# Kernel optimization log

Hardware: AMD Instinct MI355X
Metric: run time of the kernel (lower is better)

Reference implementation:

```python
import jax, jax.numpy as jnp
import numpy as np

S, B, E, H = 2048, 2, 1024, 16
D = E // H


def setup_inputs() -> dict:
    key = jax.random.key(0)
    k1, k2, k3, k4 = jax.random.split(key, 4)
    x = jax.random.normal(k1, (S, B, E), dtype=jnp.float32)
    # xavier_uniform for [3E, E] and [O, E]
    lim_qkv = float(np.sqrt(6.0 / (3 * E + E)))
    lim_out = float(np.sqrt(6.0 / (E + E)))
    w_qkv = jax.random.uniform(k2, (3 * E, E), jnp.float32, -lim_qkv, lim_qkv)
    b_qkv = jnp.zeros((3 * E,), jnp.float32)
    w_out = jax.random.uniform(k3, (E, E), jnp.float32, -lim_out, lim_out)
    b_out = jnp.zeros((E,), jnp.float32)
    return {"x": x, "w_qkv": w_qkv, "b_qkv": b_qkv, "w_out": w_out, "b_out": b_out}


def reference(x, w_qkv, b_qkv, w_out, b_out):
    # x: [S, B, E] (seq-first, as in the torch module)
    s, b, e = x.shape
    scaling = jnp.asarray(np.sqrt(D), x.dtype)
    qkv = jnp.einsum('sbe,fe->sbf', x, w_qkv) + b_qkv          # [S,B,3E]
    q, k, v = jnp.split(qkv, 3, axis=-1)
    q = q.reshape(s, b, H, D)
    k = k.reshape(s, b, H, D)
    v = v.reshape(s, b, H, D)
    # scores [B,H,S,S]; note original divides by sqrt(head_dim)
    scores = jnp.einsum('sbhd,tbhd->bhst', q, k) / scaling
    attn_w = jax.nn.softmax(scores.astype(jnp.float32), axis=-1).astype(scores.dtype)
    # dropout p=0.1 is identity in eval mode (training=False)
    attn = jnp.einsum('bhst,tbhd->sbhd', attn_w, v).reshape(s, b, e)
    out = jnp.einsum('sbe,oe->sbo', attn, w_out) + b_out        # [S,B,O]
    attn_avg = attn_w.mean(axis=1)                              # [B,S,S]
    return out, attn_avg
```

## Files before the change

### kernel.cpp

```cpp
#include <hip/hip_runtime.h>

#define SEQ   2048
#define BATCH 2
#define NH    16
#define HD    64
#define EMB   1024

#define QSCALE 0.18033688011112042f

using bf16x8 = __attribute__((ext_vector_type(8))) short;
using f32x4  = __attribute__((ext_vector_type(4))) float;
using f32x16 = __attribute__((ext_vector_type(16))) float;

__device__ __forceinline__ unsigned short f2bf(float f) {
  unsigned int u = __float_as_uint(f);
  u += 0x7FFFu + ((u >> 16) & 1u);
  return (unsigned short)(u >> 16);
}
__device__ __forceinline__ unsigned pk_bf16(float lo, float hi) {
  unsigned r;
  asm("v_cvt_pk_bf16_f32 %0, %1, %2" : "=v"(r) : "v"(lo), "v"(hi));
  return r;
}
__device__ __forceinline__ void gload16(const void* g, void* l) {
  __builtin_amdgcn_global_load_lds(
      (const __attribute__((address_space(1))) unsigned int*)g,
      (__attribute__((address_space(3))) unsigned int*)l, 16, 0, 0);
}

__global__ __launch_bounds__(256) void cvt3_f32_bf16(
    const float* __restrict__ a, int na4,
    const float* __restrict__ b, int nb4,
    const float* __restrict__ c, int nc4,
    unsigned short* __restrict__ oa,
    unsigned short* __restrict__ ob,
    unsigned short* __restrict__ oc) {
  int i = blockIdx.x * 256 + threadIdx.x;
  const float* src;
  unsigned short* dst;
  int j = i;
  if (j < na4) { src = a; dst = oa; }
  else if ((j -= na4) < nb4) { src = b; dst = ob; }
  else { j -= nb4; if (j >= nc4) return; src = c; dst = oc; }
  float4 v = reinterpret_cast<const float4*>(src)[j];
  ushort4 o;
  o.x = f2bf(v.x); o.y = f2bf(v.y); o.z = f2bf(v.z); o.w = f2bf(v.w);
  reinterpret_cast<ushort4*>(dst)[j] = o;
}

template <int EPI>
__global__ __launch_bounds__(256) void gemm_bt(
    const unsigned short* __restrict__ A,
    const unsigned short* __restrict__ B,
    const float* __restrict__ bias,
    float* __restrict__ Cf,
    unsigned short* __restrict__ Qb,
    unsigned short* __restrict__ Kb,
    unsigned short* __restrict__ VTb,
    int M, int N, int K) {
  __shared__ int4 As[128][8];
  __shared__ int4 Bs[128][8];
  const int tid = threadIdx.x;
  const int wid = tid >> 6, lane = tid & 63;
  const int wm = wid >> 1, wn = wid & 1;
  const int lg = lane >> 4, lr = lane & 15;
  const int lr8 = lane >> 3;
  const int lc8 = (lane & 7) ^ lr8;
  const int row0 = blockIdx.x * 128, col0 = blockIdx.y * 128;
  f32x4 acc[4][4] = {};
  for (int k0 = 0; k0 < K; k0 += 64) {
#pragma unroll
    for (int i = 0; i < 4; i++) {
      const int rb = wid * 32 + i * 8;
      gload16(&A[(size_t)(row0 + rb + lr8) * K + k0 + lc8 * 8], &As[rb][0]);
      gload16(&B[(size_t)(col0 + rb + lr8) * K + k0 + lc8 * 8], &Bs[rb][0]);
    }
    __syncthreads();
#pragma unroll
    for (int ks = 0; ks < 2; ks++) {
      bf16x8 af[4], bfr[4];
#pragma unroll
      for (int mi = 0; mi < 4; mi++) {
        int r = wm * 64 + mi * 16 + lr;
        af[mi] = *reinterpret_cast<const bf16x8*>(&As[r][(ks * 4 + lg) ^ (r & 7)]);
      }
#pragma unroll
      for (int ni = 0; ni < 4; ni++) {
        int r = wn * 64 + ni * 16 + lr;
        bfr[ni] = *reinterpret_cast<const bf16x8*>(&Bs[r][(ks * 4 + lg) ^ (r & 7)]);
      }
#pragma unroll
      for (int mi = 0; mi < 4; mi++)
#pragma unroll
        for (int ni = 0; ni < 4; ni++)
          acc[mi][ni] = __builtin_amdgcn_mfma_f32_16x16x32_bf16(af[mi], bfr[ni], acc[mi][ni], 0, 0, 0);
    }
    __syncthreads();
  }
#pragma unroll
  for (int mi = 0; mi < 4; mi++)
#pragma unroll
    for (int ni = 0; ni < 4; ni++) {
      const int row_b = row0 + wm * 64 + mi * 16 + lg * 4;
      const int col = col0 + wn * 64 + ni * 16 + lr;
      const float bs = bias[col];
      float v0 = acc[mi][ni][0] + bs;
      float v1 = acc[mi][ni][1] + bs;
      float v2 = acc[mi][ni][2] + bs;
      float v3 = acc[mi][ni][3] + bs;
      if (EPI == 0) {
        Cf[(size_t)(row_b + 0) * N + col] = v0;
        Cf[(size_t)(row_b + 1) * N + col] = v1;
        Cf[(size_t)(row_b + 2) * N + col] = v2;
        Cf[(size_t)(row_b + 3) * N + col] = v3;
      } else {
        const int which = col >> 10, rr = col & 1023;
        const int hh = rr >> 6, d = rr & 63;
        if (which == 2) {
          const int s0 = row_b >> 1;
          ushort2 p0; p0.x = f2bf(v0); p0.y = f2bf(v2);
          ushort2 p1; p1.x = f2bf(v1); p1.y = f2bf(v3);
          *reinterpret_cast<ushort2*>(&VTb[((size_t)((0 * NH + hh) * HD + d)) * SEQ + s0]) = p0;
          *reinterpret_cast<ushort2*>(&VTb[((size_t)((1 * NH + hh) * HD + d)) * SEQ + s0]) = p1;
        } else {
          unsigned short* dst = which == 0 ? Qb : Kb;
          const float sc = (which == 0) ? QSCALE : 1.0f;
          float vv[4] = {v0 * sc, v1 * sc, v2 * sc, v3 * sc};
#pragma unroll
          for (int r = 0; r < 4; r++) {
            int s = (row_b + r) >> 1, bb = r & 1;
            dst[(size_t)((bb * NH + hh) * SEQ + s) * HD + d] = f2bf(vv[r]);
          }
        }
      }
    }
}

__global__ __launch_bounds__(256, 2) void attn1(
    const unsigned short* __restrict__ Qb,
    const unsigned short* __restrict__ Kb,
    const unsigned short* __restrict__ VTb,
    unsigned short* __restrict__ attn_bf,
    float* __restrict__ lbuf) {
  __shared__ int4 Kt[2][64][8];
  __shared__ int4 Vt[2][64][8];
  const int tid = threadIdx.x;
  const int wid = tid >> 6, lane = tid & 63;
  const int l31 = lane & 31, lhi = lane >> 5;
  const int lr8 = lane >> 3;
  const int L = blockIdx.x;
  const int v = (L & 7) * 64 + (L >> 3);
  const int bh = v >> 4, stile = v & 15;
  const int b = bh >> 4, h = bh & 15;
  const int s0 = stile * 128 + wid * 32;
  const unsigned short* Qg = Qb + (size_t)bh * SEQ * HD;
  const unsigned short* Kg = Kb + (size_t)bh * SEQ * HD;
  const unsigned short* VTg = VTb + (size_t)bh * HD * SEQ;

  bf16x8 qf[4];
#pragma unroll
  for (int ks = 0; ks < 4; ks++)
    qf[ks] = *reinterpret_cast<const bf16x8*>(Qg + (size_t)(s0 + l31) * HD + ks * 16 + lhi * 8);

  auto stage = [&](int tg, int buf) {
#pragma unroll
    for (int i = 0; i < 2; i++) {
      const int rb = wid * 16 + i * 8;
      const int lc = (lane & 7) ^ (((rb >> 2) + lhi) & 7);
      gload16(Kg + (size_t)(tg * 64 + rb + lr8) * HD + lc * 8, &Kt[buf][rb][0]);
      gload16(VTg + (size_t)(rb + lr8) * SEQ + tg * 64 + lc * 8, &Vt[buf][rb][0]);
    }
  };
  const int swv = l31 >> 2;

  const f32x16 fz = {};
  f32x16 o[2] = {};
  f32x16 osum = {};
  const short one_bf = (short)0x3F80;
  const bf16x8 vone = {one_bf, one_bf, one_bf, one_bf, one_bf, one_bf, one_bf, one_bf};
  bf16x8 paq[4];
  bf16x8 vfr[2][4];

  auto qk = [&](int cur, f32x16 st[2]) {
#pragma unroll
    for (int ti = 0; ti < 2; ti++) {
      const int row = ti * 32 + l31;
      bf16x8 kf = *reinterpret_cast<const bf16x8*>(&Kt[cur][row][lhi ^ swv]);
      st[ti] = __builtin_amdgcn_mfma_f32_32x32x16_bf16(kf, qf[0], fz, 0, 0, 0);
    }
#pragma unroll
    for (int ks = 1; ks < 4; ks++)
#pragma unroll
      for (int ti = 0; ti < 2; ti++) {
        const int row = ti * 32 + l31;
        bf16x8 kf = *reinterpret_cast<const bf16x8*>(&Kt[cur][row][(ks * 2 + lhi) ^ swv]);
        st[ti] = __builtin_amdgcn_mfma_f32_32x32x16_bf16(kf, qf[ks], st[ti], 0, 0, 0);
      }
  };
  auto softpack = [&](const f32x16 st[2]) {
    float p[32];
#pragma unroll
    for (int ti = 0; ti < 2; ti++)
#pragma unroll
      for (int r = 0; r < 16; r++)
        p[ti * 16 + r] = __builtin_amdgcn_exp2f(st[ti][r]);
#pragma unroll
    for (int c = 0; c < 4; c++) {
      const int ti = c >> 1, cc = c & 1;
      const int pb = ti * 16 + cc * 8;
      unsigned w0 = pk_bf16(p[pb + 0], p[pb + 1]);
      unsigned w1 = pk_bf16(p[pb + 2], p[pb + 3]);
      unsigned w2 = pk_bf16(p[pb + 4], p[pb + 5]);
      unsigned w3 = pk_bf16(p[pb + 6], p[pb + 7]);
      asm volatile("v_permlane32_swap_b32 %0, %1" : "+v"(w0), "+v"(w2));
      asm volatile("v_permlane32_swap_b32 %0, %1" : "+v"(w1), "+v"(w3));
      union { unsigned u[4]; bf16x8 v; } pa;
      pa.u[0] = w0; pa.u[1] = w1; pa.u[2] = w2; pa.u[3] = w3;
      paq[c] = pa.v;
    }
  };
  auto loadv = [&](int cur) {
#pragma unroll
    for (int dt = 0; dt < 2; dt++)
#pragma unroll
      for (int c = 0; c < 4; c++) {
        const int row = dt * 32 + l31;
        vfr[dt][c] = *reinterpret_cast<const bf16x8*>(&Vt[cur][row][(c * 2 + lhi) ^ swv]);
      }
  };

  stage(0, 0);
  __syncthreads();

  {
    stage(1, 1);
    f32x16 st[2];
    __builtin_amdgcn_s_setprio(1);
    qk(0, st);
    __builtin_amdgcn_s_setprio(0);
    softpack(st);
    loadv(0);
    __syncthreads();
  }

  for (int t = 1; t < 32; t++) {
    const int cur = t & 1;
    if (t + 1 < 32) stage(t + 1, cur ^ 1);
    f32x16 st[2];
    __builtin_amdgcn_s_setprio(1);
#pragma unroll
    for (int c = 0; c < 4; c++) {
#pragma unroll
      for (int dt = 0; dt < 2; dt++)
        o[dt] = __builtin_amdgcn_mfma_f32_32x32x16_bf16(paq[c], vfr[dt][c], o[dt], 0, 0, 0);
      osum = __builtin_amdgcn_mfma_f32_32x32x16_bf16(paq[c], vone, osum, 0, 0, 0);
    }
    qk(cur, st);
    __builtin_amdgcn_s_setprio(0);
    softpack(st);
    loadv(cur);
    __syncthreads();
  }
#pragma unroll
  for (int c = 0; c < 4; c++) {
#pragma unroll
    for (int dt = 0; dt < 2; dt++)
      o[dt] = __builtin_amdgcn_mfma_f32_32x32x16_bf16(paq[c], vfr[dt][c], o[dt], 0, 0, 0);
    osum = __builtin_amdgcn_mfma_f32_32x32x16_bf16(paq[c], vone, osum, 0, 0, 0);
  }

  if (l31 == 0) {
#pragma unroll
    for (int r = 0; r < 16; r++)
      lbuf[(size_t)bh * SEQ + s0 + (r & 3) + 8 * (r >> 2) + 4 * lhi] = osum[r];
  }

#pragma unroll
  for (int r = 0; r < 16; r++) {
    float inv = __builtin_amdgcn_rcpf(osum[r]);
    const int s = s0 + (r & 3) + 8 * (r >> 2) + 4 * lhi;
#pragma unroll
    for (int dt = 0; dt < 2; dt++) {
      float ov = o[dt][r] * inv;
      attn_bf[((size_t)s * BATCH + b) * EMB + h * HD + dt * 32 + l31] = f2bf(ov);
    }
  }
}

__global__ __launch_bounds__(256, 2) void attn2(
    const unsigned short* __restrict__ Qb,
    const unsigned short* __restrict__ Kb,
    const float* __restrict__ lbuf,
    float* __restrict__ avg_out) {
  const int b = blockIdx.z;
  const int s0 = blockIdx.y * 64;
  const int tc0 = blockIdx.x * 256;
  __shared__ int4 Qs[2][64][8];
  __shared__ int4 Ks[2][2][64][8];
  __shared__ float lls[NH][64];
  const int tid = threadIdx.x;
  const int wid = tid >> 6, lane = tid & 63;
  const int wm = wid >> 1, wn = wid & 1;
  const int lg = lane >> 4, lr = lane & 15;
  const int lr8 = lane >> 3;
  const int lc8 = (lane & 7) ^ lr8;

  for (int i = tid; i < NH * 64; i += 256) {
    int hh = i >> 6, r = i & 63;
    lls[hh][r] = 1.0f / ((float)NH * lbuf[(b * NH + hh) * SEQ + s0 + r]);
  }

  const size_t bh0 = (size_t)(b * NH) * SEQ;

  auto stageK = [&](const unsigned short* src, int buf, int hsel) {
#pragma unroll
    for (int i = 0; i < 2; i++) {
      const int rb = wid * 16 + i * 8;
      gload16(src + (size_t)(rb + lr8) * HD + lc8 * 8, &Ks[buf][hsel][rb][0]);
    }
  };
  auto stageQ = [&](const unsigned short* src, int hsel) {
#pragma unroll
    for (int i = 0; i < 2; i++) {
      const int rb = wid * 16 + i * 8;
      gload16(src + (size_t)(rb + lr8) * HD + lc8 * 8, &Qs[hsel][rb][0]);
    }
  };

  stageQ(Qb + (bh0 + s0) * HD, 0);
  stageQ(Qb + (bh0 + SEQ + s0) * HD, 1);
  stageK(Kb + (bh0 + tc0) * HD, 0, 0);
  stageK(Kb + (bh0 + SEQ + tc0) * HD, 0, 1);
  __syncthreads();

  const f32x4 fz4 = {};
  f32x4 avg[4][2][2] = {};

  for (int hp = 0; hp < NH / 2; hp++) {
    const int h0 = 2 * hp, h1 = h0 + 1;
    bf16x8 af[2][2][2];
#pragma unroll
    for (int hh = 0; hh < 2; hh++)
#pragma unroll
      for (int mi = 0; mi < 2; mi++) {
        int r = wm * 32 + mi * 16 + lr;
#pragma unroll
        for (int ks = 0; ks < 2; ks++)
          af[hh][mi][ks] = *reinterpret_cast<const bf16x8*>(&Qs[hh][r][(ks * 4 + lg) ^ (r & 7)]);
      }
    float linv[2][2][4];
#pragma unroll
    for (int hh = 0; hh < 2; hh++)
#pragma unroll
      for (int mi = 0; mi < 2; mi++)
#pragma unroll
        for (int r = 0; r < 4; r++)
          linv[hh][mi][r] = lls[h0 + hh][wm * 32 + mi * 16 + lg * 4 + r];

    const unsigned short* Kg0 = Kb + (bh0 + (size_t)h0 * SEQ + tc0) * HD;
    const unsigned short* Kg1 = Kb + (bh0 + (size_t)h1 * SEQ + tc0) * HD;

    for (int t0 = 0; t0 < 4; t0++) {
      const int cur = t0 & 1;
      if (t0 < 3) {
        stageK(Kg0 + (size_t)(t0 + 1) * 64 * HD, cur ^ 1, 0);
        stageK(Kg1 + (size_t)(t0 + 1) * 64 * HD, cur ^ 1, 1);
      } else if (hp + 1 < NH / 2) {
        stageK(Kb + (bh0 + (size_t)(h0 + 2) * SEQ + tc0) * HD, cur ^ 1, 0);
        stageK(Kb + (bh0 + (size_t)(h1 + 2) * SEQ + tc0) * HD, cur ^ 1, 1);
        stageQ(Qb + (bh0 + (size_t)(h0 + 2) * SEQ + s0) * HD, 0);
        stageQ(Qb + (bh0 + (size_t)(h1 + 2) * SEQ + s0) * HD, 1);
      }
      f32x4 sacc[2][2][2];
      __builtin_amdgcn_s_setprio(1);
#pragma unroll
      for (int hh = 0; hh < 2; hh++)
#pragma unroll
        for (int ks = 0; ks < 2; ks++) {
          bf16x8 bk[2];
#pragma unroll
          for (int ni = 0; ni < 2; ni++) {
            int rk = wn * 32 + ni * 16 + lr;
            bk[ni] = *reinterpret_cast<const bf16x8*>(&Ks[cur][hh][rk][(ks * 4 + lg) ^ (rk & 7)]);
          }
#pragma unroll
          for (int mi = 0; mi < 2; mi++)
#pragma unroll
            for (int ni = 0; ni < 2; ni++)
              sacc[hh][mi][ni] = __builtin_amdgcn_mfma_f32_16x16x32_bf16(
                  af[hh][mi][ks], bk[ni], ks == 0 ? fz4 : sacc[hh][mi][ni], 0, 0, 0);
        }
      __builtin_amdgcn_s_setprio(0);
#pragma unroll
      for (int hh = 0; hh < 2; hh++)
#pragma unroll
        for (int mi = 0; mi < 2; mi++)
#pragma unroll
          for (int ni = 0; ni < 2; ni++)
#pragma unroll
            for (int r = 0; r < 4; r++)
              avg[t0][mi][ni][r] += __builtin_amdgcn_exp2f(sacc[hh][mi][ni][r]) * linv[hh][mi][r];
      __syncthreads();
    }
  }

#pragma unroll
  for (int t0 = 0; t0 < 4; t0++)
#pragma unroll
    for (int mi = 0; mi < 2; mi++)
#pragma unroll
      for (int ni = 0; ni < 2; ni++)
#pragma unroll
        for (int r = 0; r < 4; r++) {
          int s = s0 + wm * 32 + mi * 16 + lg * 4 + r;
          int t = tc0 + t0 * 64 + wn * 32 + ni * 16 + lr;
          avg_out[((size_t)b * SEQ + s) * SEQ + t] = avg[t0][mi][ni][r];
        }
}

extern "C" void kernel_launch(void* const* d_in, const int* in_sizes, int n_in,
                              void* d_out, int out_size, void* d_ws, size_t ws_size,
                              hipStream_t stream) {
  const float* x     = (const float*)d_in[0];
  const float* w_qkv = (const float*)d_in[1];
  const float* b_qkv = (const float*)d_in[2];
  const float* w_out = (const float*)d_in[3];
  const float* b_out = (const float*)d_in[4];
  float* out = (float*)d_out;
  float* avg = out + (size_t)SEQ * BATCH * EMB;

  char* ws = (char*)d_ws;
  size_t off = 0;
  unsigned short* x_bf    = (unsigned short*)(ws + off); off += (size_t)SEQ * BATCH * EMB * 2;
  unsigned short* wqkv_bf = (unsigned short*)(ws + off); off += (size_t)3 * EMB * EMB * 2;
  unsigned short* wout_bf = (unsigned short*)(ws + off); off += (size_t)EMB * EMB * 2;
  unsigned short* Qbuf    = (unsigned short*)(ws + off); off += (size_t)BATCH * NH * SEQ * HD * 2;
  unsigned short* Kbuf    = (unsigned short*)(ws + off); off += (size_t)BATCH * NH * SEQ * HD * 2;
  unsigned short* VTbuf   = (unsigned short*)(ws + off); off += (size_t)BATCH * NH * HD * SEQ * 2;
  unsigned short* attn_bf = (unsigned short*)(ws + off); off += (size_t)SEQ * BATCH * EMB * 2;
  float*          lbuf    = (float*)(ws + off);          off += (size_t)BATCH * NH * SEQ * 4;

  {
    const int na4 = SEQ * BATCH * EMB / 4;
    const int nb4 = 3 * EMB * EMB / 4;
    const int nc4 = EMB * EMB / 4;
    const int nblk = (na4 + nb4 + nc4 + 255) / 256;
    cvt3_f32_bf16<<<nblk, 256, 0, stream>>>(x, na4, w_qkv, nb4, w_out, nc4,
                                            x_bf, wqkv_bf, wout_bf);
  }

  gemm_bt<1><<<dim3(SEQ * BATCH / 128, 3 * EMB / 128), 256, 0, stream>>>(
      x_bf, wqkv_bf, b_qkv, nullptr, Qbuf, Kbuf, VTbuf, SEQ * BATCH, 3 * EMB, EMB);

  attn1<<<512, 256, 0, stream>>>(Qbuf, Kbuf, VTbuf, attn_bf, lbuf);

  attn2<<<dim3(SEQ / 256, SEQ / 64, BATCH), 256, 0, stream>>>(Qbuf, Kbuf, lbuf, avg);

  gemm_bt<0><<<dim3(SEQ * BATCH / 128, EMB / 128), 256, 0, stream>>>(
      attn_bf, wout_bf, b_out, out, nullptr, nullptr, nullptr, SEQ * BATCH, EMB, EMB);
}
```

Before: 145.0 us.

## Merge out-projection GEMM and attention-average kernel into one launch

Combines the output-projection GEMM and the attention-weight averaging kernel into a single launch. The first 256 blocks do the GEMM and the remaining blocks compute the head-averaged probabilities, sharing one raw shared-memory buffer. Both depend only on attn1's outputs, so they can now run at the same time, filling the GPU and removing a launch and the tail idle time between them. The cost is a larger shared-memory footprint per block and dropping the 2-blocks-per-CU launch bound for the average path, which may reduce occupancy.

```diff
diff --git a/kernel.cpp b/kernel.cpp
--- a/kernel.cpp
+++ b/kernel.cpp
@@ -48,12 +48,10 @@
   reinterpret_cast<ushort4*>(dst)[j] = o;
 }
 
-template <int EPI>
-__global__ __launch_bounds__(256) void gemm_bt(
+__global__ __launch_bounds__(256) void gemm_qkv(
     const unsigned short* __restrict__ A,
     const unsigned short* __restrict__ B,
     const float* __restrict__ bias,
-    float* __restrict__ Cf,
     unsigned short* __restrict__ Qb,
     unsigned short* __restrict__ Kb,
     unsigned short* __restrict__ VTb,
@@ -108,29 +106,22 @@
       float v1 = acc[mi][ni][1] + bs;
       float v2 = acc[mi][ni][2] + bs;
       float v3 = acc[mi][ni][3] + bs;
-      if (EPI == 0) {
-        Cf[(size_t)(row_b + 0) * N + col] = v0;
-        Cf[(size_t)(row_b + 1) * N + col] = v1;
-        Cf[(size_t)(row_b + 2) * N + col] = v2;
-        Cf[(size_t)(row_b + 3) * N + col] = v3;
+      const int which = col >> 10, rr = col & 1023;
+      const int hh = rr >> 6, d = rr & 63;
+      if (which == 2) {
+        const int s0 = row_b >> 1;
+        ushort2 p0; p0.x = f2bf(v0); p0.y = f2bf(v2);
+        ushort2 p1; p1.x = f2bf(v1); p1.y = f2bf(v3);
+        *reinterpret_cast<ushort2*>(&VTb[((size_t)((0 * NH + hh) * HD + d)) * SEQ + s0]) = p0;
+        *reinterpret_cast<ushort2*>(&VTb[((size_t)((1 * NH + hh) * HD + d)) * SEQ + s0]) = p1;
       } else {
-        const int which = col >> 10, rr = col & 1023;
-        const int hh = rr >> 6, d = rr & 63;
-        if (which == 2) {
-          const int s0 = row_b >> 1;
-          ushort2 p0; p0.x = f2bf(v0); p0.y = f2bf(v2);
-          ushort2 p1; p1.x = f2bf(v1); p1.y = f2bf(v3);
-          *reinterpret_cast<ushort2*>(&VTb[((size_t)((0 * NH + hh) * HD + d)) * SEQ + s0]) = p0;
-          *reinterpret_cast<ushort2*>(&VTb[((size_t)((1 * NH + hh) * HD + d)) * SEQ + s0]) = p1;
-        } else {
-          unsigned short* dst = which == 0 ? Qb : Kb;
-          const float sc = (which == 0) ? QSCALE : 1.0f;
-          float vv[4] = {v0 * sc, v1 * sc, v2 * sc, v3 * sc};
-#pragma unroll
-          for (int r = 0; r < 4; r++) {
-            int s = (row_b + r) >> 1, bb = r & 1;
-            dst[(size_t)((bb * NH + hh) * SEQ + s) * HD + d] = f2bf(vv[r]);
-          }
+        unsigned short* dst = which == 0 ? Qb : Kb;
+        const float sc = (which == 0) ? QSCALE : 1.0f;
+        float vv[4] = {v0 * sc, v1 * sc, v2 * sc, v3 * sc};
+#pragma unroll
+        for (int r = 0; r < 4; r++) {
+          int s = (row_b + r) >> 1, bb = r & 1;
+          dst[(size_t)((bb * NH + hh) * SEQ + s) * HD + d] = f2bf(vv[r]);
         }
       }
     }
@@ -287,17 +278,17 @@
   }
 }
 
-__global__ __launch_bounds__(256, 2) void attn2(
+#define TAIL_GEMM_BLOCKS 256
+__global__ __launch_bounds__(256) void tail_fused(
+    const unsigned short* __restrict__ attn_bf,
+    const unsigned short* __restrict__ wout_bf,
+    const float* __restrict__ b_out,
+    float* __restrict__ out,
     const unsigned short* __restrict__ Qb,
     const unsigned short* __restrict__ Kb,
     const float* __restrict__ lbuf,
     float* __restrict__ avg_out) {
-  const int b = blockIdx.z;
-  const int s0 = blockIdx.y * 64;
-  const int tc0 = blockIdx.x * 256;
-  __shared__ int4 Qs[2][64][8];
-  __shared__ int4 Ks[2][2][64][8];
-  __shared__ float lls[NH][64];
+  __shared__ __align__(16) char smem[53248];
   const int tid = threadIdx.x;
   const int wid = tid >> 6, lane = tid & 63;
   const int wm = wid >> 1, wn = wid & 1;
@@ -305,117 +296,175 @@
   const int lr8 = lane >> 3;
   const int lc8 = (lane & 7) ^ lr8;
 
-  for (int i = tid; i < NH * 64; i += 256) {
-    int hh = i >> 6, r = i & 63;
-    lls[hh][r] = 1.0f / ((float)NH * lbuf[(b * NH + hh) * SEQ + s0 + r]);
-  }
-
-  const size_t bh0 = (size_t)(b * NH) * SEQ;
-
-  auto stageK = [&](const unsigned short* src, int buf, int hsel) {
-#pragma unroll
-    for (int i = 0; i < 2; i++) {
-      const int rb = wid * 16 + i * 8;
-      gload16(src + (size_t)(rb + lr8) * HD + lc8 * 8, &Ks[buf][hsel][rb][0]);
-    }
-  };
-  auto stageQ = [&](const unsigned short* src, int hsel) {
-#pragma unroll
-    for (int i = 0; i < 2; i++) {
-      const int rb = wid * 16 + i * 8;
-      gload16(src + (size_t)(rb + lr8) * HD + lc8 * 8, &Qs[hsel][rb][0]);
-    }
-  };
-
-  stageQ(Qb + (bh0 + s0) * HD, 0);
-  stageQ(Qb + (bh0 + SEQ + s0) * HD, 1);
-  stageK(Kb + (bh0 + tc0) * HD, 0, 0);
-  stageK(Kb + (bh0 + SEQ + tc0) * HD, 0, 1);
-  __syncthreads();
-
-  const f32x4 fz4 = {};
-  f32x4 avg[4][2][2] = {};
-
-  for (int hp = 0; hp < NH / 2; hp++) {
-    const int h0 = 2 * hp, h1 = h0 + 1;
-    bf16x8 af[2][2][2];
-#pragma unroll
-    for (int hh = 0; hh < 2; hh++)
-#pragma unroll
-      for (int mi = 0; mi < 2; mi++) {
-        int r = wm * 32 + mi * 16 + lr;
-#pragma unroll
-        for (int ks = 0; ks < 2; ks++)
-          af[hh][mi][ks] = *reinterpret_cast<const bf16x8*>(&Qs[hh][r][(ks * 4 + lg) ^ (r & 7)]);
-      }
-    float linv[2][2][4];
-#pragma unroll
-    for (int hh = 0; hh < 2; hh++)
+  if (blockIdx.x < TAIL_GEMM_BLOCKS) {
+    const int id = blockIdx.x;
+    const int row0 = (id & 31) * 128, col0 = (id >> 5) * 128;
+    int4 (*As)[8] = reinterpret_cast<int4(*)[8]>(smem);
+    int4 (*Bs)[8] = reinterpret_cast<int4(*)[8]>(smem + 16384);
+    const int K = EMB, N = EMB;
+    f32x4 acc[4][4] = {};
+    for (int k0 = 0; k0 < K; k0 += 64) {
+#pragma unroll
+      for (int i = 0; i < 4; i++) {
+        const int rb = wid * 32 + i * 8;
+        gload16(&attn_bf[(size_t)(row0 + rb + lr8) * K + k0 + lc8 * 8], &As[rb][0]);
+        gload16(&wout_bf[(size_t)(col0 + rb + lr8) * K + k0 + lc8 * 8], &Bs[rb][0]);
+      }
+      __syncthreads();
+#pragma unroll
+      for (int ks = 0; ks < 2; ks++) {
+        bf16x8 af[4], bfr[4];
+#pragma unroll
+        for (int mi = 0; mi < 4; mi++) {
+          int r = wm * 64 + mi * 16 + lr;
+          af[mi] = *reinterpret_cast<const bf16x8*>(&As[r][(ks * 4 + lg) ^ (r & 7)]);
+        }
+#pragma unroll
+        for (int ni = 0; ni < 4; ni++) {
+          int r = wn * 64 + ni * 16 + lr;
+          bfr[ni] = *reinterpret_cast<const bf16x8*>(&Bs[r][(ks * 4 + lg) ^ (r & 7)]);
+        }
+#pragma unroll
+        for (int mi = 0; mi < 4; mi++)
+#pragma unroll
+          for (int ni = 0; ni < 4; ni++)
+            acc[mi][ni] = __builtin_amdgcn_mfma_f32_16x16x32_bf16(af[mi], bfr[ni], acc[mi][ni], 0, 0, 0);
+      }
+      __syncthreads();
+    }
+#pragma unroll
+    for (int mi = 0; mi < 4; mi++)
+#pragma unroll
+      for (int ni = 0; ni < 4; ni++) {
+        const int row_b = row0 + wm * 64 + mi * 16 + lg * 4;
+        const int col = col0 + wn * 64 + ni * 16 + lr;
+        const float bs = b_out[col];
+        out[(size_t)(row_b + 0) * N + col] = acc[mi][ni][0] + bs;
+        out[(size_t)(row_b + 1) * N + col] = acc[mi][ni][1] + bs;
+        out[(size_t)(row_b + 2) * N + col] = acc[mi][ni][2] + bs;
+        out[(size_t)(row_b + 3) * N + col] = acc[mi][ni][3] + bs;
+      }
+  } else {
+    const int a = blockIdx.x - TAIL_GEMM_BLOCKS;
+    const int b = a >> 8;
+    const int s0 = ((a >> 3) & 31) * 64;
+    const int tc0 = (a & 7) * 256;
+    int4 (*Qs)[64][8] = reinterpret_cast<int4(*)[64][8]>(smem);
+    int4 (*Ks)[2][64][8] = reinterpret_cast<int4(*)[2][64][8]>(smem + 16384);
+    float (*lls)[64] = reinterpret_cast<float(*)[64]>(smem + 49152);
+
+    for (int i = tid; i < NH * 64; i += 256) {
+      int hh = i >> 6, r = i & 63;
+      lls[hh][r] = 1.0f / ((float)NH * lbuf[(b * NH + hh) * SEQ + s0 + r]);
+    }
+
+    const size_t bh0 = (size_t)(b * NH) * SEQ;
+
+    auto stageK = [&](const unsigned short* src, int buf, int hsel) {
+#pragma unroll
+      for (int i = 0; i < 2; i++) {
+        const int rb = wid * 16 + i * 8;
+        gload16(src + (size_t)(rb + lr8) * HD + lc8 * 8, &Ks[buf][hsel][rb][0]);
+      }
+    };
+    auto stageQ = [&](const unsigned short* src, int hsel) {
+#pragma unroll
+      for (int i = 0; i < 2; i++) {
+        const int rb = wid * 16 + i * 8;
+        gload16(src + (size_t)(rb + lr8) * HD + lc8 * 8, &Qs[hsel][rb][0]);
+      }
+    };
+
+    stageQ(Qb + (bh0 + s0) * HD, 0);
+    stageQ(Qb + (bh0 + SEQ + s0) * HD, 1);
+    stageK(Kb + (bh0 + tc0) * HD, 0, 0);
+    stageK(Kb + (bh0 + SEQ + tc0) * HD, 0, 1);
+    __syncthreads();
+
+    const f32x4 fz4 = {};
+    f32x4 avg[4][2][2] = {};
+
+    for (int hp = 0; hp < NH / 2; hp++) {
+      const int h0 = 2 * hp, h1 = h0 + 1;
+      bf16x8 af[2][2][2];
+#pragma unroll
+      for (int hh = 0; hh < 2; hh++)
+#pragma unroll
+        for (int mi = 0; mi < 2; mi++) {
+          int r = wm * 32 + mi * 16 + lr;
+#pragma unroll
+          for (int ks = 0; ks < 2; ks++)
+            af[hh][mi][ks] = *reinterpret_cast<const bf16x8*>(&Qs[hh][r][(ks * 4 + lg) ^ (r & 7)]);
+        }
+      float linv[2][2][4];
+#pragma unroll
+      for (int hh = 0; hh < 2; hh++)
+#pragma unroll
+        for (int mi = 0; mi < 2; mi++)
+#pragma unroll
+          for (int r = 0; r < 4; r++)
+            linv[hh][mi][r] = lls[h0 + hh][wm * 32 + mi * 16 + lg * 4 + r];
+
+      const unsigned short* Kg0 = Kb + (bh0 + (size_t)h0 * SEQ + tc0) * HD;
+      const unsigned short* Kg1 = Kb + (bh0 + (size_t)h1 * SEQ + tc0) * HD;
+
+      for (int t0 = 0; t0 < 4; t0++) {
+        const int cur = t0 & 1;
+        if (t0 < 3) {
+          stageK(Kg0 + (size_t)(t0 + 1) * 64 * HD, cur ^ 1, 0);
+          stageK(Kg1 + (size_t)(t0 + 1) * 64 * HD, cur ^ 1, 1);
+        } else if (hp + 1 < NH / 2) {
+          stageK(Kb + (bh0 + (size_t)(h0 + 2) * SEQ + tc0) * HD, cur ^ 1, 0);
+          stageK(Kb + (bh0 + (size_t)(h1 + 2) * SEQ + tc0) * HD, cur ^ 1, 1);
+          stageQ(Qb + (bh0 + (size_t)(h0 + 2) * SEQ + s0) * HD, 0);
+          stageQ(Qb + (bh0 + (size_t)(h1 + 2) * SEQ + s0) * HD, 1);
+        }
+        f32x4 sacc[2][2][2];
+        __builtin_amdgcn_s_setprio(1);
+#pragma unroll
+        for (int hh = 0; hh < 2; hh++)
+#pragma unroll
+          for (int ks = 0; ks < 2; ks++) {
+            bf16x8 bk[2];
+#pragma unroll
+            for (int ni = 0; ni < 2; ni++) {
+              int rk = wn * 32 + ni * 16 + lr;
+              bk[ni] = *reinterpret_cast<const bf16x8*>(&Ks[cur][hh][rk][(ks * 4 + lg) ^ (rk & 7)]);
+            }
+#pragma unroll
+            for (int mi = 0; mi < 2; mi++)
+#pragma unroll
+              for (int ni = 0; ni < 2; ni++)
+                sacc[hh][mi][ni] = __builtin_amdgcn_mfma_f32_16x16x32_bf16(
+                    af[hh][mi][ks], bk[ni], ks == 0 ? fz4 : sacc[hh][mi][ni], 0, 0, 0);
+          }
+        __builtin_amdgcn_s_setprio(0);
+#pragma unroll
+        for (int hh = 0; hh < 2; hh++)
+#pragma unroll
+          for (int mi = 0; mi < 2; mi++)
+#pragma unroll
+            for (int ni = 0; ni < 2; ni++)
+#pragma unroll
+              for (int r = 0; r < 4; r++)
+                avg[t0][mi][ni][r] += __builtin_amdgcn_exp2f(sacc[hh][mi][ni][r]) * linv[hh][mi][r];
+        __syncthreads();
+      }
+    }
+
+#pragma unroll
+    for (int t0 = 0; t0 < 4; t0++)
 #pragma unroll
       for (int mi = 0; mi < 2; mi++)
 #pragma unroll
-        for (int r = 0; r < 4; r++)
-          linv[hh][mi][r] = lls[h0 + hh][wm * 32 + mi * 16 + lg * 4 + r];
-
-    const unsigned short* Kg0 = Kb + (bh0 + (size_t)h0 * SEQ + tc0) * HD;
-    const unsigned short* Kg1 = Kb + (bh0 + (size_t)h1 * SEQ + tc0) * HD;
-
-    for (int t0 = 0; t0 < 4; t0++) {
-      const int cur = t0 & 1;
-      if (t0 < 3) {
-        stageK(Kg0 + (size_t)(t0 + 1) * 64 * HD, cur ^ 1, 0);
-        stageK(Kg1 + (size_t)(t0 + 1) * 64 * HD, cur ^ 1, 1);
-      } else if (hp + 1 < NH / 2) {
-        stageK(Kb + (bh0 + (size_t)(h0 + 2) * SEQ + tc0) * HD, cur ^ 1, 0);
-        stageK(Kb + (bh0 + (size_t)(h1 + 2) * SEQ + tc0) * HD, cur ^ 1, 1);
-        stageQ(Qb + (bh0 + (size_t)(h0 + 2) * SEQ + s0) * HD, 0);
-        stageQ(Qb + (bh0 + (size_t)(h1 + 2) * SEQ + s0) * HD, 1);
-      }
-      f32x4 sacc[2][2][2];
-      __builtin_amdgcn_s_setprio(1);
-#pragma unroll
-      for (int hh = 0; hh < 2; hh++)
-#pragma unroll
-        for (int ks = 0; ks < 2; ks++) {
-          bf16x8 bk[2];
-#pragma unroll
-          for (int ni = 0; ni < 2; ni++) {
-            int rk = wn * 32 + ni * 16 + lr;
-            bk[ni] = *reinterpret_cast<const bf16x8*>(&Ks[cur][hh][rk][(ks * 4 + lg) ^ (rk & 7)]);
+        for (int ni = 0; ni < 2; ni++)
+#pragma unroll
+          for (int r = 0; r < 4; r++) {
+            int s = s0 + wm * 32 + mi * 16 + lg * 4 + r;
+            int t = tc0 + t0 * 64 + wn * 32 + ni * 16 + lr;
+            avg_out[((size_t)b * SEQ + s) * SEQ + t] = avg[t0][mi][ni][r];
           }
-#pragma unroll
-          for (int mi = 0; mi < 2; mi++)
-#pragma unroll
-            for (int ni = 0; ni < 2; ni++)
-              sacc[hh][mi][ni] = __builtin_amdgcn_mfma_f32_16x16x32_bf16(
-                  af[hh][mi][ks], bk[ni], ks == 0 ? fz4 : sacc[hh][mi][ni], 0, 0, 0);
-        }
-      __builtin_amdgcn_s_setprio(0);
-#pragma unroll
-      for (int hh = 0; hh < 2; hh++)
-#pragma unroll
-        for (int mi = 0; mi < 2; mi++)
-#pragma unroll
-          for (int ni = 0; ni < 2; ni++)
-#pragma unroll
-            for (int r = 0; r < 4; r++)
-              avg[t0][mi][ni][r] += __builtin_amdgcn_exp2f(sacc[hh][mi][ni][r]) * linv[hh][mi][r];
-      __syncthreads();
-    }
-  }
-
-#pragma unroll
-  for (int t0 = 0; t0 < 4; t0++)
-#pragma unroll
-    for (int mi = 0; mi < 2; mi++)
-#pragma unroll
-      for (int ni = 0; ni < 2; ni++)
-#pragma unroll
-        for (int r = 0; r < 4; r++) {
-          int s = s0 + wm * 32 + mi * 16 + lg * 4 + r;
-          int t = tc0 + t0 * 64 + wn * 32 + ni * 16 + lr;
-          avg_out[((size_t)b * SEQ + s) * SEQ + t] = avg[t0][mi][ni][r];
-        }
+  }
 }
 
 extern "C" void kernel_launch(void* const* d_in, const int* in_sizes, int n_in,
@@ -449,13 +498,11 @@
                                             x_bf, wqkv_bf, wout_bf);
   }
 
-  gemm_bt<1><<<dim3(SEQ * BATCH / 128, 3 * EMB / 128), 256, 0, stream>>>(
-      x_bf, wqkv_bf, b_qkv, nullptr, Qbuf, Kbuf, VTbuf, SEQ * BATCH, 3 * EMB, EMB);
+  gemm_qkv<<<dim3(SEQ * BATCH / 128, 3 * EMB / 128), 256, 0, stream>>>(
+      x_bf, wqkv_bf, b_qkv, Qbuf, Kbuf, VTbuf, SEQ * BATCH, 3 * EMB, EMB);
 
   attn1<<<512, 256, 0, stream>>>(Qbuf, Kbuf, VTbuf, attn_bf, lbuf);
 
-  attn2<<<dim3(SEQ / 256, SEQ / 64, BATCH), 256, 0, stream>>>(Qbuf, Kbuf, lbuf, avg);
-
-  gemm_bt<0><<<dim3(SEQ * BATCH / 128, EMB / 128), 256, 0, stream>>>(
-      attn_bf, wout_bf, b_out, out, nullptr, nullptr, nullptr, SEQ * BATCH, EMB, EMB);
-}
+  tail_fused<<<TAIL_GEMM_BLOCKS + SEQ / 256 * SEQ / 64 * BATCH, 256, 0, stream>>>(
+      attn_bf, wout_bf, b_out, out, Qbuf, Kbuf, lbuf, avg);
+}
```

Result: slower. 155.8 us (+7.4%).
